# Performance work log

Hardware: AMD Instinct MI355X
Metric: run time of the kernel (lower is better)

The kernel has to match this reference:

```python
import jax, jax.numpy as jnp
import numpy as np

B, T, I, H = 64, 512, 512, 1024

def setup_inputs() -> dict:
    key = jax.random.key(0)
    k1, k2, k3 = jax.random.split(key, 3)
    x = jax.random.normal(k1, (B, T, I), dtype=jnp.float32)
    # kaiming_normal_(nonlinearity='relu'): std = sqrt(2/fan_in)
    Wi = jax.random.normal(k2, (H, I), dtype=jnp.float32) * np.sqrt(2.0 / I)
    Wh = jax.random.normal(k3, (H, H), dtype=jnp.float32) * np.sqrt(2.0 / H)
    bi = jnp.zeros((H,), dtype=jnp.float32)
    bh = jnp.zeros((H,), dtype=jnp.float32)
    return {"x": x, "Wi": Wi, "bi": bi, "Wh": Wh, "bh": bh}

def reference(x, Wi, bi, Wh, bh):
    # batch_first=True: x is [B,T,I]; internally process time-major [T,B,I]
    xt = jnp.transpose(x, (1, 0, 2))  # [T,B,I]
    # precompute input projection for all steps in one GEMM
    pre = jnp.einsum('tbi,hi->tbh', xt, Wi) + bi + bh  # [T,B,H]

    def step(h, p_t):
        h = jax.nn.relu(p_t + h @ Wh.T)  # [B,H]
        return h, h

    h0 = jnp.zeros((x.shape[0], Wh.shape[0]), dtype=x.dtype)
    hidden, outs = jax.lax.scan(step, h0, pre)  # outs: [T,B,H]
    output = jnp.transpose(outs, (1, 0, 2))  # [B,T,H]
    return (output, hidden)
```

## Files before the change

### kernel.cpp

```cpp
#include <hip/hip_runtime.h>

#define B_ 64
#define T_ 512
#define I_ 512
#define H_ 1024
#define FPAD 16
#define TPS 16384
#define NWG 256

typedef __attribute__((ext_vector_type(8))) short bf16x8;
typedef __attribute__((ext_vector_type(4))) float f32x4;

static __device__ __forceinline__ short f2bf(float f) {
  unsigned u = __float_as_uint(f);
  unsigned r = (u + 0x7fffu + ((u >> 16) & 1u)) >> 16;
  return (short)(unsigned short)r;
}
static __device__ __forceinline__ float bf2f(short s) {
  return __uint_as_float(((unsigned)(unsigned short)s) << 16);
}
static __device__ __forceinline__ bf16x8 pack8(float4 u, float4 v) {
  bf16x8 r;
  r[0] = f2bf(u.x); r[1] = f2bf(u.y); r[2] = f2bf(u.z); r[3] = f2bf(u.w);
  r[4] = f2bf(v.x); r[5] = f2bf(v.y); r[6] = f2bf(v.z); r[7] = f2bf(v.w);
  return r;
}

#define PBK 32
#define PLDA 40

__global__ __launch_bounds__(256) void proj_gemm(
    const float* __restrict__ x, const float* __restrict__ Wi,
    const float* __restrict__ bi, const float* __restrict__ bh,
    float* __restrict__ out) {
  __shared__ short As[128 * PLDA];
  __shared__ short Bs[128 * PLDA];
  const int tid = threadIdx.x;
  const int m0 = (blockIdx.x >> 3) * 128;
  const int n0 = (blockIdx.x & 7) * 128;
  const int wave = tid >> 6, lane = tid & 63;
  const int wm = (wave & 1) * 64, wn = (wave >> 1) * 64;
  const int lm = lane & 15, lq = lane >> 4;

  f32x4 acc[4][4];
#pragma unroll
  for (int i = 0; i < 4; ++i)
#pragma unroll
    for (int j = 0; j < 4; ++j) {
      f32x4 z = {0.f, 0.f, 0.f, 0.f};
      acc[i][j] = z;
    }

  const int lrow = tid >> 1;
  const int lcol = (tid & 1) * 16;
  const float* xp = x + (size_t)(m0 + lrow) * I_ + lcol;
  const float* wp = Wi + (size_t)(n0 + lrow) * I_ + lcol;

  for (int k0 = 0; k0 < I_; k0 += PBK) {
    float4 a0 = *(const float4*)(xp + k0);
    float4 a1 = *(const float4*)(xp + k0 + 4);
    float4 a2 = *(const float4*)(xp + k0 + 8);
    float4 a3 = *(const float4*)(xp + k0 + 12);
    float4 b0 = *(const float4*)(wp + k0);
    float4 b1 = *(const float4*)(wp + k0 + 4);
    float4 b2 = *(const float4*)(wp + k0 + 8);
    float4 b3 = *(const float4*)(wp + k0 + 12);
    __syncthreads();
    *(bf16x8*)&As[lrow * PLDA + lcol] = pack8(a0, a1);
    *(bf16x8*)&As[lrow * PLDA + lcol + 8] = pack8(a2, a3);
    *(bf16x8*)&Bs[lrow * PLDA + lcol] = pack8(b0, b1);
    *(bf16x8*)&Bs[lrow * PLDA + lcol + 8] = pack8(b2, b3);
    __syncthreads();

    bf16x8 af[4], bfr[4];
#pragma unroll
    for (int i = 0; i < 4; ++i)
      af[i] = *(const bf16x8*)&As[(wm + i * 16 + lm) * PLDA + lq * 8];
#pragma unroll
    for (int j = 0; j < 4; ++j)
      bfr[j] = *(const bf16x8*)&Bs[(wn + j * 16 + lm) * PLDA + lq * 8];
#pragma unroll
    for (int i = 0; i < 4; ++i)
#pragma unroll
      for (int j = 0; j < 4; ++j)
        acc[i][j] = __builtin_amdgcn_mfma_f32_16x16x32_bf16(af[i], bfr[j],
                                                            acc[i][j], 0, 0, 0);
  }

  const int rb = m0 + wm + lq * 4;
  const int cb = n0 + wn + lm;
#pragma unroll
  for (int j = 0; j < 4; ++j) {
    const int n = cb + j * 16;
    const float bias = bi[n] + bh[n];
#pragma unroll
    for (int i = 0; i < 4; ++i) {
      const int m = rb + i * 16;
#pragma unroll
      for (int r = 0; r < 4; ++r)
        out[(size_t)(m + r) * H_ + n] = acc[i][j][r] + bias;
    }
  }
}

static __device__ __forceinline__ unsigned long long ld_a8(const void* p) {
  return __hip_atomic_load((const unsigned long long*)p, __ATOMIC_RELAXED,
                           __HIP_MEMORY_SCOPE_AGENT);
}
static __device__ __forceinline__ void st_a2(unsigned short* p,
                                             unsigned short v) {
  __hip_atomic_store(p, v, __ATOMIC_RELAXED, __HIP_MEMORY_SCOPE_AGENT);
}
static __device__ __forceinline__ int ld_flag(const int* p) {
  return __hip_atomic_load(p, __ATOMIC_RELAXED, __HIP_MEMORY_SCOPE_AGENT);
}

union frag_u {
  unsigned long long q[2];
  bf16x8 v;
};

__global__ __launch_bounds__(256, 1) void rnn_rec(
    const float* __restrict__ Wh, float* __restrict__ out,
    unsigned short* __restrict__ planes, int* __restrict__ flags) {
  const int tid = threadIdx.x;
  const int wg = blockIdx.x;
  const int team = wg >> 6;
  const int w = wg & 63;
  const int wv = tid >> 6;
  const int lane = tid & 63;
  const int lm = lane & 15, lq = lane >> 4;

  bf16x8 Bh[8], Bl[8];
  {
    const float* wrow = Wh + (size_t)(16 * w + lm) * H_ + wv * 256 + lq * 8;
#pragma unroll
    for (int i = 0; i < 8; ++i) {
      const int kbl = (w + i) & 7;
      float4 w0 = *(const float4*)(wrow + kbl * 32);
      float4 w1 = *(const float4*)(wrow + kbl * 32 + 4);
      float wf[8] = {w0.x, w0.y, w0.z, w0.w, w1.x, w1.y, w1.z, w1.w};
      bf16x8 hi, lo;
#pragma unroll
      for (int j = 0; j < 8; ++j) {
        hi[j] = f2bf(wf[j]);
        lo[j] = f2bf(wf[j] - bf2f(hi[j]));
      }
      Bh[i] = hi;
      Bl[i] = lo;
    }
  }

  const int r = tid >> 4;
  const int cl = tid & 15;
  const int c = 16 * w + cl;
  const int b = team * 16 + r;
  const int Sidx = (c >> 5) * 512 + ((c >> 3) & 3) * 128 + r * 8 + (c & 7);

  unsigned short* tbase = planes + (size_t)team * 4 * TPS;
  const int* frd = flags + (team * 64 + 16 * wv + lm) * FPAD;
  const int* fwr = flags + (team * 64 + lane) * FPAD;
  const int fown = wg * FPAD;

  st_a2(tbase + Sidx, 0);
  st_a2(tbase + TPS + Sidx, 0);
  asm volatile("s_waitcnt vmcnt(0)" ::: "memory");
  __syncthreads();
  if (tid == 0)
    __hip_atomic_store(&flags[fown], 0, __ATOMIC_RELAXED,
                       __HIP_MEMORY_SCOPE_AGENT);

  float* outH = out + (size_t)B_ * T_ * H_;
  __shared__ float red[4][64][4];
  const int lp = (r >> 2) * 16 + cl;
  const int ri = r & 3;

  for (int s = 1; s <= T_; ++s) {
    const int t = s - 1;
    const size_t oidx = (size_t)b * (T_ * H_) + (size_t)t * H_ + c;
    const float pre = out[oidx];

    const int need = s - 1;
    for (;;) {
      const int f = ld_flag(frd);
      if (__all(f >= need)) break;
      __builtin_amdgcn_s_sleep(1);
    }

    const char* src = (const char*)(tbase + (size_t)((s - 1) & 1) * 2 * TPS);
    unsigned long long q[8][4];
#pragma unroll
    for (int i = 0; i < 8; ++i) {
      const int kb = 8 * wv + ((w + i) & 7);
      const char* p = src + kb * 1024 + lane * 16;
      q[i][0] = ld_a8(p);
      q[i][1] = ld_a8(p + 8);
      q[i][2] = ld_a8(p + 32768);
      q[i][3] = ld_a8(p + 32768 + 8);
    }

    const f32x4 z = {0.f, 0.f, 0.f, 0.f};
    f32x4 c0 = z, c1 = z, c2 = z;
#pragma unroll
    for (int i = 0; i < 8; ++i) {
      frag_u ah, al;
      ah.q[0] = q[i][0];
      ah.q[1] = q[i][1];
      al.q[0] = q[i][2];
      al.q[1] = q[i][3];
      c0 = __builtin_amdgcn_mfma_f32_16x16x32_bf16(ah.v, Bh[i], c0, 0, 0, 0);
      c1 = __builtin_amdgcn_mfma_f32_16x16x32_bf16(ah.v, Bl[i], c1, 0, 0, 0);
      c2 = __builtin_amdgcn_mfma_f32_16x16x32_bf16(al.v, Bh[i], c2, 0, 0, 0);
    }
    const f32x4 rs = c0 + c1 + c2;

    *(f32x4*)&red[wv][lane][0] = rs;
    for (;;) {
      const int f = ld_flag(fwr);
      if (__all(f >= need)) break;
      __builtin_amdgcn_s_sleep(1);
    }
    __syncthreads();
    const float sum = red[0][lp][ri] + red[1][lp][ri] + red[2][lp][ri] +
                      red[3][lp][ri];
    float v = pre + sum;
    v = v > 0.f ? v : 0.f;

    unsigned short* dst = tbase + (size_t)(s & 1) * 2 * TPS;
    const short hv = f2bf(v);
    const short lv = f2bf(v - bf2f(hv));
    st_a2(dst + Sidx, (unsigned short)hv);
    st_a2(dst + TPS + Sidx, (unsigned short)lv);
    asm volatile("s_waitcnt vmcnt(0)" ::: "memory");
    __syncthreads();
    if (tid == 0)
      __hip_atomic_store(&flags[fown], s, __ATOMIC_RELAXED,
                         __HIP_MEMORY_SCOPE_AGENT);

    out[oidx] = v;
    if (s == T_) outH[(size_t)b * H_ + c] = v;
  }
}

extern "C" void kernel_launch(void* const* d_in, const int* in_sizes, int n_in,
                              void* d_out, int out_size, void* d_ws,
                              size_t ws_size, hipStream_t stream) {
  const float* x = (const float*)d_in[0];
  const float* Wi = (const float*)d_in[1];
  const float* bi = (const float*)d_in[2];
  const float* Wh = (const float*)d_in[3];
  const float* bh = (const float*)d_in[4];
  float* out = (float*)d_out;

  int* flags = (int*)d_ws;
  unsigned short* planes =
      (unsigned short*)((char*)d_ws + NWG * FPAD * 4);

  proj_gemm<<<2048, 256, 0, stream>>>(x, Wi, bi, bh, out);
  rnn_rec<<<NWG, 256, 0, stream>>>(Wh, out, planes, flags);
}
```

Before: 2.773 ms.

## Deepen hidden-state ring to four buffers and pack stores through LDS

Replaces the double-buffered hidden-state exchange with a four-deep ring. Writers now wait only until consumers are within three steps instead of one, which loosens the write-after-read synchronization between workgroups. The per-thread 2-byte atomic stores are replaced by an LDS repack, after which one wave issues 8-byte atomic stores for the hi and lo planes. The output stores move ahead of the flag publish. The cost is an extra __syncthreads and an LDS round trip on the critical path each step, plus a larger workspace.

```diff
diff --git a/kernel.cpp b/kernel.cpp
--- a/kernel.cpp
+++ b/kernel.cpp
@@ -7,6 +7,9 @@
 #define FPAD 16
 #define TPS 16384
 #define NWG 256
+#define PAIRB 65536
+#define NDEPTH 4
+#define TEAMB (NDEPTH * PAIRB)
 
 typedef __attribute__((ext_vector_type(8))) short bf16x8;
 typedef __attribute__((ext_vector_type(4))) float f32x4;
@@ -111,6 +114,10 @@
                                              unsigned short v) {
   __hip_atomic_store(p, v, __ATOMIC_RELAXED, __HIP_MEMORY_SCOPE_AGENT);
 }
+static __device__ __forceinline__ void st_a8(unsigned long long* p,
+                                             unsigned long long v) {
+  __hip_atomic_store(p, v, __ATOMIC_RELAXED, __HIP_MEMORY_SCOPE_AGENT);
+}
 static __device__ __forceinline__ int ld_flag(const int* p) {
   return __hip_atomic_load(p, __ATOMIC_RELAXED, __HIP_MEMORY_SCOPE_AGENT);
 }
@@ -122,7 +129,7 @@
 
 __global__ __launch_bounds__(256, 1) void rnn_rec(
     const float* __restrict__ Wh, float* __restrict__ out,
-    unsigned short* __restrict__ planes, int* __restrict__ flags) {
+    char* __restrict__ planes, int* __restrict__ flags) {
   const int tid = threadIdx.x;
   const int wg = blockIdx.x;
   const int team = wg >> 6;
@@ -155,15 +162,18 @@
   const int cl = tid & 15;
   const int c = 16 * w + cl;
   const int b = team * 16 + r;
-  const int Sidx = (c >> 5) * 512 + ((c >> 3) & 3) * 128 + r * 8 + (c & 7);
-
-  unsigned short* tbase = planes + (size_t)team * 4 * TPS;
+  const int Sidx = 256 * w + (cl >> 3) * 128 + r * 8 + (cl & 7);
+
+  char* tbase = planes + (size_t)team * TEAMB;
   const int* frd = flags + (team * 64 + 16 * wv + lm) * FPAD;
   const int* fwr = flags + (team * 64 + lane) * FPAD;
   const int fown = wg * FPAD;
 
-  st_a2(tbase + Sidx, 0);
-  st_a2(tbase + TPS + Sidx, 0);
+  {
+    unsigned short* p0 = (unsigned short*)tbase;
+    st_a2(p0 + Sidx, 0);
+    st_a2(p0 + TPS + Sidx, 0);
+  }
   asm volatile("s_waitcnt vmcnt(0)" ::: "memory");
   __syncthreads();
   if (tid == 0)
@@ -172,8 +182,11 @@
 
   float* outH = out + (size_t)B_ * T_ * H_;
   __shared__ float red[4][64][4];
+  __shared__ unsigned pk[16][17];
   const int lp = (r >> 2) * 16 + cl;
   const int ri = r & 3;
+  const int pr = (lane >> 1) & 15;
+  const int pc0 = (lane >> 5) * 8 + (lane & 1) * 4;
 
   for (int s = 1; s <= T_; ++s) {
     const int t = s - 1;
@@ -187,7 +200,7 @@
       __builtin_amdgcn_s_sleep(1);
     }
 
-    const char* src = (const char*)(tbase + (size_t)((s - 1) & 1) * 2 * TPS);
+    const char* src = tbase + (size_t)((s - 1) & 3) * PAIRB;
     unsigned long long q[8][4];
 #pragma unroll
     for (int i = 0; i < 8; ++i) {
@@ -215,9 +228,10 @@
     const f32x4 rs = c0 + c1 + c2;
 
     *(f32x4*)&red[wv][lane][0] = rs;
+    const int need2 = s - 3;
     for (;;) {
       const int f = ld_flag(fwr);
-      if (__all(f >= need)) break;
+      if (__all(f >= need2)) break;
       __builtin_amdgcn_s_sleep(1);
     }
     __syncthreads();
@@ -226,19 +240,30 @@
     float v = pre + sum;
     v = v > 0.f ? v : 0.f;
 
-    unsigned short* dst = tbase + (size_t)(s & 1) * 2 * TPS;
     const short hv = f2bf(v);
     const short lv = f2bf(v - bf2f(hv));
-    st_a2(dst + Sidx, (unsigned short)hv);
-    st_a2(dst + TPS + Sidx, (unsigned short)lv);
-    asm volatile("s_waitcnt vmcnt(0)" ::: "memory");
+    pk[r][cl] = (unsigned)(unsigned short)hv | ((unsigned)(unsigned short)lv << 16);
+    out[oidx] = v;
+    if (s == T_) outH[(size_t)b * H_ + c] = v;
+    __syncthreads();
+
+    if (wv == 0) {
+      unsigned long long hq = 0, lq2 = 0;
+#pragma unroll
+      for (int k = 0; k < 4; ++k) {
+        const unsigned u = pk[pr][pc0 + k];
+        hq |= ((unsigned long long)(u & 0xffffu)) << (16 * k);
+        lq2 |= ((unsigned long long)(u >> 16)) << (16 * k);
+      }
+      char* dst = tbase + (size_t)(s & 3) * PAIRB;
+      st_a8((unsigned long long*)(dst + 512 * w + 8 * lane), hq);
+      st_a8((unsigned long long*)(dst + 32768 + 512 * w + 8 * lane), lq2);
+      asm volatile("s_waitcnt vmcnt(0)" ::: "memory");
+    }
     __syncthreads();
     if (tid == 0)
       __hip_atomic_store(&flags[fown], s, __ATOMIC_RELAXED,
                          __HIP_MEMORY_SCOPE_AGENT);
-
-    out[oidx] = v;
-    if (s == T_) outH[(size_t)b * H_ + c] = v;
   }
 }
 
@@ -253,8 +278,7 @@
   float* out = (float*)d_out;
 
   int* flags = (int*)d_ws;
-  unsigned short* planes =
-      (unsigned short*)((char*)d_ws + NWG * FPAD * 4);
+  char* planes = (char*)d_ws + 32768;
 
   proj_gemm<<<2048, 256, 0, stream>>>(x, Wi, bi, bh, out);
   rnn_rec<<<NWG, 256, 0, stream>>>(Wh, out, planes, flags);
```

Measured after the change: 2.724 ms. Within noise of the previous version (-1.8%).
